# Kernel optimization log

Measured on AMD Instinct MI355X. Metric: run time of the kernel, lower is better.

## Reference

```python
import jax, jax.numpy as jnp
import numpy as np

BINS = 5
POINTS = 2
EPS_DIV = 1e-6
GN_GROUPS = 32
GN_EPS = 1e-5


def bilinear_sum(img, ys, xs):
    """Sum of bilinear samples with zero padding outside the image.
    img: (B, C, H, W); ys, xs: (B, K, H, W) absolute sample coords.
    Returns (B, C, H, W) = sum over K of bilinear(img, ys_k, xs_k)."""
    B, C, H, W = img.shape
    K = ys.shape[1]
    y0 = jnp.floor(ys)
    x0 = jnp.floor(xs)
    imgf = img.reshape(B, C, H * W)
    acc = jnp.zeros((B, C, K, H, W), img.dtype)
    for dy, dx in ((0, 0), (0, 1), (1, 0), (1, 1)):
        yi = y0 + dy
        xi = x0 + dx
        w = (1.0 - jnp.abs(ys - yi)) * (1.0 - jnp.abs(xs - xi))
        valid = (yi >= 0) & (yi <= H - 1) & (xi >= 0) & (xi <= W - 1)
        yc = jnp.clip(yi, 0, H - 1).astype(jnp.int32)
        xc = jnp.clip(xi, 0, W - 1).astype(jnp.int32)
        idx = (yc * W + xc).reshape(B, 1, K * H * W)
        g = jnp.take_along_axis(imgf, idx, axis=2).reshape(B, C, K, H, W)
        acc = acc + (w * valid.astype(img.dtype))[:, None] * g
    return acc.sum(axis=2)


def setup_inputs():
    key = jax.random.key(0)
    ks = jax.random.split(key, 6)
    B, C, H, W = 2, 256, 100, 152
    P, K = POINTS, BINS
    x = jax.random.normal(ks[0], (B, C, H, W), jnp.float32)
    offsets = jax.random.normal(ks[1], (B, P * K * 2, H, W), jnp.float32) * 2.0
    ef_w = jax.random.normal(ks[2], (P * C, C), jnp.float32) * 0.02
    ef_b = jnp.zeros((P * C,), jnp.float32)
    hm1_w = jax.random.normal(ks[3], (P, C, C), jnp.float32) * 0.02
    hm1_b = jnp.zeros((P, C), jnp.float32)
    hm2_w = jax.random.normal(ks[4], (P, C), jnp.float32) * 0.02
    hm2_b = jnp.zeros((P,), jnp.float32)
    merge_w = jax.random.normal(ks[5], (C, P * C), jnp.float32) * 0.02
    merge_b = jnp.zeros((C,), jnp.float32)
    gn_g = jnp.ones((C,), jnp.float32)
    gn_b = jnp.zeros((C,), jnp.float32)
    return {"x": x, "offsets": offsets, "ef_w": ef_w, "ef_b": ef_b,
            "hm1_w": hm1_w, "hm1_b": hm1_b, "hm2_w": hm2_w, "hm2_b": hm2_b,
            "merge_w": merge_w, "merge_b": merge_b, "gn_g": gn_g, "gn_b": gn_b}


def reference(x, offsets, ef_w, ef_b, hm1_w, hm1_b, hm2_w, hm2_b, merge_w, merge_b, gn_g, gn_b):
    B, C, H, W = x.shape
    P, K = POINTS, BINS
    # expand_feat: 1x1 conv C -> P*C
    ef = jnp.einsum('bchw,dc->bdhw', x, ef_w) + ef_b[None, :, None, None]
    efp = ef.reshape(B, P, C, H, W)
    # heatmap: grouped 1x1 conv (per-point) -> ReLU -> grouped 1x1 conv -> exp
    h = jax.nn.relu(jnp.einsum('bpchw,pdc->bpdhw', efp, hm1_w) + hm1_b[None, :, :, None, None])
    heat = jnp.exp(jnp.einsum('bpdhw,pd->bphw', h, hm2_w) + hm2_b[None, :, None, None])  # (B,P,H,W)
    # offsets: (B, P, K, 2, H, W) with channel layout [y, x] per bin.
    # base_offset cancels the [1,bins] kernel grid, so the deform conv with
    # all-ones weights is simply: sum over bins of bilinear samples at
    # (h + off_y, w + off_x).
    off = offsets.reshape(B, P, K, 2, H, W)
    hg = jnp.arange(H, dtype=x.dtype)[None, None, None, :, None]
    wg = jnp.arange(W, dtype=x.dtype)[None, None, None, None, :]
    ys = hg + off[:, :, :, 0]  # (B,P,K,H,W)
    xs = wg + off[:, :, :, 1]
    outs = []
    for p in range(P):
        # sample feat*heat (C channels) and heat (1 channel) together
        img = jnp.concatenate([efp[:, p] * heat[:, p][:, None], heat[:, p][:, None]], axis=1)
        s = bilinear_sum(img, ys[:, p], xs[:, p])  # (B, C+1, H, W)
        outs.append(s[:, :C] / (s[:, C:] + EPS_DIV))
    outs = jnp.concatenate(outs, axis=1)  # (B, P*C, H, W)
    merged = jnp.einsum('bchw,dc->bdhw', outs, merge_w) + merge_b[None, :, None, None]
    # GroupNorm(32, C) + ReLU
    g = merged.reshape(B, GN_GROUPS, C // GN_GROUPS, H, W)
    mu = g.mean(axis=(2, 3, 4), keepdims=True)
    var = g.var(axis=(2, 3, 4), keepdims=True)
    gn = ((g - mu) / jnp.sqrt(var + GN_EPS)).reshape(B, C, H, W)
    gn = gn * gn_g[None, :, None, None] + gn_b[None, :, None, None]
    return jax.nn.relu(gn)
```

## Files before the change

### kernel.cpp

```cpp
#include <hip/hip_runtime.h>

#define BINS 5
#define PTS  2
constexpr int Bx = 2, Cc = 256, Hh = 100, Ww = 152;
constexpr int HW = Hh * Ww;
constexpr int NTILE = 238;
constexpr float EPS_DIV = 1e-6f;
constexpr float GN_EPS  = 1e-5f;

typedef __attribute__((ext_vector_type(8))) _Float16 hfrag;
typedef __attribute__((ext_vector_type(2))) _Float16 h2;
typedef __attribute__((ext_vector_type(4))) float f32x4;

__device__ __forceinline__ ushort f2h(float f) {
    return __builtin_bit_cast(ushort, (_Float16)f);
}
__device__ __forceinline__ float hlo(unsigned u) {
    return (float)__builtin_bit_cast(_Float16, (ushort)(u & 0xffffu));
}
__device__ __forceinline__ float hhi(unsigned u) {
    return (float)__builtin_bit_cast(_Float16, (ushort)(u >> 16));
}

#define GLL16(g, l) __builtin_amdgcn_global_load_lds( \
    (const __attribute__((address_space(1))) unsigned*)(g), \
    (__attribute__((address_space(3))) unsigned*)(l), 16, 0, 0)

__global__ __launch_bounds__(256)
void k_wconv(const float* __restrict__ efw, const float* __restrict__ w1,
             const float* __restrict__ mw, ushort* __restrict__ wb)
{
    int gid = blockIdx.x * 256 + threadIdx.x;
    int e = gid * 4;
    int arr = e >> 17, off = e & 131071;
    const float* src = arr == 0 ? efw : (arr == 1 ? w1 : mw);
    float4 v = *(const float4*)(src + off);
    ushort4 o = { f2h(v.x), f2h(v.y), f2h(v.z), f2h(v.w) };
    *(ushort4*)(wb + e) = o;
}

__global__ __launch_bounds__(256)
void k_xt(const float* __restrict__ x, ushort* __restrict__ xbt)
{
    __shared__ float tile[32][33];
    const int t = threadIdx.x;
    const int hw0 = blockIdx.x * 32;
    const int c0 = blockIdx.y * 32;
    const int b = blockIdx.z;
    const float* xb = x + ((size_t)b * Cc + c0) * HW + hw0;
    const int tx = t & 31, ty = t >> 5;
    #pragma unroll
    for (int r = 0; r < 4; r++) {
        int c = ty + r * 8;
        tile[c][tx] = xb[(size_t)c * HW + tx];
    }
    __syncthreads();
    const int hwl = t >> 3, c4 = (t & 7) * 4;
    ushort4 o = { f2h(tile[c4 + 0][hwl]), f2h(tile[c4 + 1][hwl]),
                  f2h(tile[c4 + 2][hwl]), f2h(tile[c4 + 3][hwl]) };
    *(ushort4*)&xbt[((size_t)b * HW + hw0 + hwl) * Cc + c0 + c4] = o;
}

__global__ __launch_bounds__(512)
void k_ef(const ushort* __restrict__ xbt, const ushort* __restrict__ wbe,
          const float* __restrict__ efb, ushort* __restrict__ efp)
{
    __shared__ ushort Alds[128 * 256];
    __shared__ ushort Bl0[64 * 256];
    __shared__ ushort Bl1[64 * 256];
    const int t  = threadIdx.x;
    const int wv = t >> 6, ln = t & 63;
    const int quad = ln >> 4, l16 = ln & 15;
    const int mwv = wv & 3, ngr = wv >> 2;
    const int xr = l16 & 7;
    const int bx = blockIdx.x;
    const int n0 = blockIdx.y;
    const int b  = blockIdx.z;
    const ushort* xb = xbt + (size_t)b * HW * Cc;
    const ushort* wA = wbe + (size_t)n0 * 128 * 256;
    const int ntl = (237 - bx) / 30 + 1;

    #pragma unroll
    for (int j = 0; j < 8; j++) {
        int unit = j * 512 + t;
        int row = unit >> 5, c8 = unit & 31;
        const ushort* g = wA + row * 256 + ((c8 ^ (row & 7)) << 3);
        ushort* l = Alds + (j * 512 + wv * 64) * 8;
        GLL16(g, l);
    }
    auto stageB = [&](int tt, ushort* dst) {
        int tp0 = tt * 64;
        #pragma unroll
        for (int j = 0; j < 4; j++) {
            int unit = j * 512 + t;
            int prow = unit >> 5, c8 = unit & 31;
            int pq = tp0 + prow; if (pq > HW - 1) pq = HW - 1;
            const ushort* g = xb + (size_t)pq * 256 + ((c8 ^ (prow & 7)) << 3);
            ushort* l = dst + (j * 512 + wv * 64) * 8;
            GLL16(g, l);
        }
    };
    stageB(bx, Bl0);
    stageB(bx + 30, Bl1);
    asm volatile("s_waitcnt vmcnt(4)" ::: "memory");
    __builtin_amdgcn_s_barrier();
    __builtin_amdgcn_sched_barrier(0);

    float bias[2][4];
    #pragma unroll
    for (int dt = 0; dt < 2; dt++)
        #pragma unroll
        for (int r = 0; r < 4; r++)
            bias[dt][r] = efb[n0 * 128 + mwv * 32 + dt * 16 + quad * 4 + r];

    const int aof0 = (mwv * 32 + l16) * 256;
    const int aof1 = (mwv * 32 + 16 + l16) * 256;
    const int bof0 = (ngr * 32 + l16) * 256;
    const int bof1 = (ngr * 32 + 16 + l16) * 256;
    const int p_ = n0 >> 1;
    const int cb = (n0 & 1) * 128 + mwv * 32;
    ushort* outb = efp + (size_t)((b * PTS + p_) * HW) * Cc;

    for (int it = 0; it < ntl; it++) {
        const int tp0 = (bx + it * 30) * 64;
        const ushort* bb = (it & 1) ? Bl1 : Bl0;
        f32x4 acc[2][2];
        #pragma unroll
        for (int i = 0; i < 2; i++)
            #pragma unroll
            for (int j = 0; j < 2; j++) acc[i][j] = (f32x4){0.f, 0.f, 0.f, 0.f};
        #pragma unroll
        for (int s = 0; s < 8; s++) {
            const int co = (((s * 4 + quad) ^ xr) << 3);
            hfrag a0 = *(const hfrag*)&Alds[aof0 + co];
            hfrag a1 = *(const hfrag*)&Alds[aof1 + co];
            hfrag b0 = *(const hfrag*)&bb[bof0 + co];
            hfrag b1 = *(const hfrag*)&bb[bof1 + co];
            acc[0][0] = __builtin_amdgcn_mfma_f32_16x16x32_f16(a0, b0, acc[0][0], 0, 0, 0);
            acc[0][1] = __builtin_amdgcn_mfma_f32_16x16x32_f16(a0, b1, acc[0][1], 0, 0, 0);
            acc[1][0] = __builtin_amdgcn_mfma_f32_16x16x32_f16(a1, b0, acc[1][0], 0, 0, 0);
            acc[1][1] = __builtin_amdgcn_mfma_f32_16x16x32_f16(a1, b1, acc[1][1], 0, 0, 0);
        }
        #pragma unroll
        for (int dt = 0; dt < 2; dt++)
            #pragma unroll
            for (int pt = 0; pt < 2; pt++) {
                int pix = tp0 + ngr * 32 + pt * 16 + l16;
                if (pix < HW) {
                    ushort4 o = { f2h(acc[dt][pt][0] + bias[dt][0]),
                                  f2h(acc[dt][pt][1] + bias[dt][1]),
                                  f2h(acc[dt][pt][2] + bias[dt][2]),
                                  f2h(acc[dt][pt][3] + bias[dt][3]) };
                    *(ushort4*)&outb[(size_t)pix * Cc + cb + dt * 16 + quad * 4] = o;
                }
            }
        if (it + 1 < ntl) {
            __builtin_amdgcn_s_barrier();
            if (it + 2 < ntl) {
                stageB(bx + (it + 2) * 30, (it & 1) ? Bl1 : Bl0);
                asm volatile("s_waitcnt vmcnt(4)" ::: "memory");
            } else {
                asm volatile("s_waitcnt vmcnt(0)" ::: "memory");
            }
            __builtin_amdgcn_s_barrier();
            __builtin_amdgcn_sched_barrier(0);
        }
    }
}

__global__ __launch_bounds__(512)
void k_heat(const ushort* __restrict__ efp, const ushort* __restrict__ wb1,
            const float* __restrict__ b1, const float* __restrict__ w2,
            float* __restrict__ hp)
{
    __shared__ ushort Alds[128 * 256];
    __shared__ ushort Bl0[64 * 256];
    __shared__ ushort Bl1[64 * 256];
    __shared__ float red[2][4][32];
    const int t  = threadIdx.x;
    const int wv = t >> 6, ln = t & 63;
    const int quad = ln >> 4, l16 = ln & 15;
    const int mwv = wv & 3, ngr = wv >> 2;
    const int xr = l16 & 7;
    const int bx = blockIdx.x;
    const int p  = blockIdx.y >> 1;
    const int n0 = blockIdx.y & 1;
    const int b  = blockIdx.z;
    const ushort* eb = efp + (size_t)((b * PTS + p) * HW) * Cc;
    const ushort* wA = wb1 + (size_t)p * Cc * Cc + (size_t)n0 * 128 * 256;
    const int ntl = (237 - bx) / 30 + 1;

    #pragma unroll
    for (int j = 0; j < 8; j++) {
        int unit = j * 512 + t;
        int row = unit >> 5, c8 = unit & 31;
        const ushort* g = wA + row * 256 + ((c8 ^ (row & 7)) << 3);
        ushort* l = Alds + (j * 512 + wv * 64) * 8;
        GLL16(g, l);
    }
    auto stageB = [&](int tt, ushort* dst) {
        int tp0 = tt * 64;
        #pragma unroll
        for (int j = 0; j < 4; j++) {
            int unit = j * 512 + t;
            int prow = unit >> 5, c8 = unit & 31;
            int pq = tp0 + prow; if (pq > HW - 1) pq = HW - 1;
            const ushort* g = eb + (size_t)pq * 256 + ((c8 ^ (prow & 7)) << 3);
            ushort* l = dst + (j * 512 + wv * 64) * 8;
            GLL16(g, l);
        }
    };
    stageB(bx, Bl0);
    stageB(bx + 30, Bl1);
    asm volatile("s_waitcnt vmcnt(4)" ::: "memory");
    __builtin_amdgcn_s_barrier();
    __builtin_amdgcn_sched_barrier(0);

    const float* b1p = b1 + p * 256;
    const float* w2p = w2 + p * 256;
    float b1v[2][4], w2v[2][4];
    #pragma unroll
    for (int dt = 0; dt < 2; dt++)
        #pragma unroll
        for (int r = 0; r < 4; r++) {
            int gch = n0 * 128 + mwv * 32 + dt * 16 + quad * 4 + r;
            b1v[dt][r] = b1p[gch];
            w2v[dt][r] = w2p[gch];
        }

    const int aof0 = (mwv * 32 + l16) * 256;
    const int aof1 = (mwv * 32 + 16 + l16) * 256;
    const int bof0 = (ngr * 32 + l16) * 256;
    const int bof1 = (ngr * 32 + 16 + l16) * 256;
    float* hpo = hp + (size_t)n0 * (Bx * PTS * HW) + (size_t)(b * PTS + p) * HW;

    for (int it = 0; it < ntl; it++) {
        const int tp0 = (bx + it * 30) * 64;
        const ushort* bb = (it & 1) ? Bl1 : Bl0;
        f32x4 acc[2][2];
        #pragma unroll
        for (int i = 0; i < 2; i++)
            #pragma unroll
            for (int j = 0; j < 2; j++) acc[i][j] = (f32x4){0.f, 0.f, 0.f, 0.f};
        #pragma unroll
        for (int s = 0; s < 8; s++) {
            const int co = (((s * 4 + quad) ^ xr) << 3);
            hfrag a0 = *(const hfrag*)&Alds[aof0 + co];
            hfrag a1 = *(const hfrag*)&Alds[aof1 + co];
            hfrag b0 = *(const hfrag*)&bb[bof0 + co];
            hfrag b1f = *(const hfrag*)&bb[bof1 + co];
            acc[0][0] = __builtin_amdgcn_mfma_f32_16x16x32_f16(a0, b0, acc[0][0], 0, 0, 0);
            acc[0][1] = __builtin_amdgcn_mfma_f32_16x16x32_f16(a0, b1f, acc[0][1], 0, 0, 0);
            acc[1][0] = __builtin_amdgcn_mfma_f32_16x16x32_f16(a1, b0, acc[1][0], 0, 0, 0);
            acc[1][1] = __builtin_amdgcn_mfma_f32_16x16x32_f16(a1, b1f, acc[1][1], 0, 0, 0);
        }
        float s0 = 0.f, s1 = 0.f;
        #pragma unroll
        for (int dt = 0; dt < 2; dt++)
            #pragma unroll
            for (int r = 0; r < 4; r++) {
                float h0 = acc[dt][0][r] + b1v[dt][r];
                float h1 = acc[dt][1][r] + b1v[dt][r];
                h0 = h0 > 0.f ? h0 : 0.f;
                h1 = h1 > 0.f ? h1 : 0.f;
                s0 += w2v[dt][r] * h0;
                s1 += w2v[dt][r] * h1;
            }
        s0 += __shfl_xor(s0, 16); s0 += __shfl_xor(s0, 32);
        s1 += __shfl_xor(s1, 16); s1 += __shfl_xor(s1, 32);
        if (ln < 16) {
            red[ngr][mwv][ln]      = s0;
            red[ngr][mwv][16 + ln] = s1;
        }
        asm volatile("s_waitcnt lgkmcnt(0)" ::: "memory");
        __builtin_amdgcn_s_barrier();
        if (t < 64) {
            int g = t >> 5, i32 = t & 31;
            float v = red[g][0][i32] + red[g][1][i32] + red[g][2][i32] + red[g][3][i32];
            int pix = tp0 + t;
            if (pix < HW) hpo[pix] = v;
        }
        if (it + 1 < ntl) {
            if (it + 2 < ntl) {
                stageB(bx + (it + 2) * 30, (it & 1) ? Bl1 : Bl0);
                asm volatile("s_waitcnt vmcnt(4)" ::: "memory");
            } else {
                asm volatile("s_waitcnt vmcnt(0)" ::: "memory");
            }
            __builtin_amdgcn_s_barrier();
            __builtin_amdgcn_sched_barrier(0);
        }
    }
}

__global__ __launch_bounds__(256)
void k_hexp(const float* __restrict__ hp, const float* __restrict__ b2,
            float* __restrict__ heat)
{
    int t4 = blockIdx.x * 256 + threadIdx.x;
    if (t4 >= (Bx * PTS * HW) / 4) return;
    int i = t4 * 4;
    float b2v = b2[(i / HW) & 1];
    float4 a = *(const float4*)(hp + i);
    float4 c = *(const float4*)(hp + (size_t)(Bx * PTS * HW) + i);
    float4 o;
    o.x = expf(a.x + c.x + b2v);
    o.y = expf(a.y + c.y + b2v);
    o.z = expf(a.z + c.z + b2v);
    o.w = expf(a.w + c.w + b2v);
    *(float4*)(heat + i) = o;
}

__global__ __launch_bounds__(256)
void k_sample(const ushort* __restrict__ efp, const float* __restrict__ heat,
              const float* __restrict__ offs, ushort* __restrict__ outs)
{
    __shared__ uint2 s_wo[32][20];
    const int t = threadIdx.x;
    const int bid = blockIdx.x;
    const int nx = (bid & 7) * 60 + (bid >> 3);
    if (nx >= 475) return;
    const int m0 = nx * 32;
    const int p = blockIdx.y;
    const int b = blockIdx.z;
    const float* heat_bp = heat + (size_t)(b * PTS + p) * HW;

    if (t < 32 * BINS) {
        int j = t / BINS, k = t % BINS;
        int hw = m0 + j;
        int hh = hw / Ww, ww = hw % Ww;
        int chy = (p * BINS + k) * 2;
        float oy = offs[((size_t)b * (PTS * BINS * 2) + chy)     * HW + hw];
        float ox = offs[((size_t)b * (PTS * BINS * 2) + chy + 1) * HW + hw];
        float ysf = (float)hh + oy;
        float xsf = (float)ww + ox;
        float y0 = floorf(ysf), x0 = floorf(xsf);
        #pragma unroll
        for (int dy = 0; dy < 2; dy++)
            #pragma unroll
            for (int dx = 0; dx < 2; dx++) {
                float yi = y0 + dy, xi = x0 + dx;
                float wgt = (1.f - fabsf(ysf - yi)) * (1.f - fabsf(xsf - xi));
                bool valid = (yi >= 0.f) && (yi <= (float)(Hh - 1)) &&
                             (xi >= 0.f) && (xi <= (float)(Ww - 1));
                int yc = (int)yi; yc = yc < 0 ? 0 : (yc > Hh - 1 ? Hh - 1 : yc);
                int xc = (int)xi; xc = xc < 0 ? 0 : (xc > Ww - 1 ? Ww - 1 : xc);
                int idx = yc * Ww + xc;
                float wh = valid ? wgt * heat_bp[idx] : 0.f;
                s_wo[j][k * 4 + dy * 2 + dx] =
                    make_uint2(__float_as_uint(wh), (unsigned)idx << 9);
            }
    }
    __syncthreads();
    if (t < 32) {
        float s = 0.f;
        #pragma unroll
        for (int u = 0; u < 20; u++) s += __uint_as_float(s_wo[t][u].x);
        float inv = 1.f / (s + EPS_DIV);
        #pragma unroll
        for (int u = 0; u < 20; u++) {
            float w = __uint_as_float(s_wo[t][u].x) * inv;
            unsigned hw16 = (unsigned)f2h(w);
            s_wo[t][u].x = hw16 | (hw16 << 16);
        }
    }
    __syncthreads();

    const int wv = t >> 6, ln = t & 63;
    const int half = ln >> 5, c8 = ln & 31;
    const char* efbase = (const char*)(efp + (size_t)((b * PTS + p) * HW) * Cc)
                         + c8 * 16;
    ushort* ob = outs + ((size_t)(b * HW + m0)) * (PTS * Cc) + p * Cc + c8 * 8;
    #pragma unroll
    for (int i = 0; i < 8; i += 2) {
        const int j = wv * 8 + i + half;
        h2 a0 = (h2){0, 0}, a1 = (h2){0, 0}, a2 = (h2){0, 0}, a3 = (h2){0, 0};
        #pragma unroll
        for (int u = 0; u < 20; u++) {
            uint2 wo = s_wo[j][u];
            uint4 v = *(const uint4*)(efbase + wo.y);
            h2 wp = __builtin_bit_cast(h2, wo.x);
            a0 += wp * __builtin_bit_cast(h2, v.x);
            a1 += wp * __builtin_bit_cast(h2, v.y);
            a2 += wp * __builtin_bit_cast(h2, v.z);
            a3 += wp * __builtin_bit_cast(h2, v.w);
        }
        uint4 o = { __builtin_bit_cast(unsigned, a0), __builtin_bit_cast(unsigned, a1),
                    __builtin_bit_cast(unsigned, a2), __builtin_bit_cast(unsigned, a3) };
        *(uint4*)(ob + (size_t)j * (PTS * Cc)) = o;
    }
}

__global__ __launch_bounds__(256)
void k_merge(const ushort* __restrict__ outs, const ushort* __restrict__ wbm,
             const float* __restrict__ mb, ushort* __restrict__ mgb,
             float* __restrict__ part2)
{
    __shared__ ushort As[64 * 72];
    __shared__ ushort Bs[64 * 72];
    const int t = threadIdx.x;
    const int wv = t >> 6, ln = t & 63;
    const int quad = ln >> 4, l16 = ln & 15;
    const int pix0 = blockIdx.x * 64;
    const int n0 = blockIdx.y * 64;
    const int b = blockIdx.z;
    const ushort* ob = outs + (size_t)b * HW * (PTS * Cc);

    f32x4 acc[4];
    #pragma unroll
    for (int j = 0; j < 4; j++) acc[j] = (f32x4){0.f, 0.f, 0.f, 0.f};

    const int srow = t >> 3, scol = (t & 7) * 8;

    for (int k0 = 0; k0 < 512; k0 += 64) {
        #pragma unroll
        for (int r = 0; r < 2; r++) {
            int row = srow + r * 32;
            *(uint4*)&As[row * 72 + scol] =
                *(const uint4*)&wbm[(size_t)(n0 + row) * 512 + k0 + scol];
        }
        #pragma unroll
        for (int r = 0; r < 2; r++) {
            int row = srow + r * 32;
            int pq = pix0 + row; if (pq > HW - 1) pq = HW - 1;
            *(uint4*)&Bs[row * 72 + scol] =
                *(const uint4*)&ob[(size_t)pq * (PTS * Cc) + k0 + scol];
        }
        __syncthreads();
        #pragma unroll
        for (int kk = 0; kk < 64; kk += 32) {
            hfrag af = *(const hfrag*)&As[(wv * 16 + l16) * 72 + kk + quad * 8];
            #pragma unroll
            for (int pt = 0; pt < 4; pt++) {
                hfrag bfr = *(const hfrag*)&Bs[(pt * 16 + l16) * 72 + kk + quad * 8];
                acc[pt] = __builtin_amdgcn_mfma_f32_16x16x32_f16(
                    af, bfr, acc[pt], 0, 0, 0);
            }
        }
        __syncthreads();
    }

    const int ch = n0 + wv * 16 + quad * 4;
    float bias[4];
    #pragma unroll
    for (int r = 0; r < 4; r++) bias[r] = mb[ch + r];

    float sacc = 0.f, qacc = 0.f;
    #pragma unroll
    for (int pt = 0; pt < 4; pt++) {
        int pix = pix0 + pt * 16 + l16;
        if (pix < HW) {
            #pragma unroll
            for (int r = 0; r < 4; r++) {
                float v = acc[pt][r] + bias[r];
                mgb[((size_t)b * Cc + ch + r) * HW + pix] = f2h(v);
                sacc += v; qacc += v * v;
            }
        }
    }
    #pragma unroll
    for (int off = 1; off <= 16; off <<= 1) {
        sacc += __shfl_xor(sacc, off);
        qacc += __shfl_xor(qacc, off);
    }
    if ((ln & 31) == 0) {
        int g = (n0 >> 3) + wv * 2 + (quad >> 1);
        size_t idx = ((size_t)(b * 32 + g) * NTILE + blockIdx.x) * 2;
        part2[idx + 0] = sacc;
        part2[idx + 1] = qacc;
    }
}

__global__ __launch_bounds__(256)
void k_gnfinal(const float* __restrict__ part2, float* __restrict__ statf)
{
    const int bg = blockIdx.x;
    const int t = threadIdx.x;
    float s = 0.f, q = 0.f;
    if (t < NTILE) {
        s = part2[((size_t)bg * NTILE + t) * 2 + 0];
        q = part2[((size_t)bg * NTILE + t) * 2 + 1];
    }
    #pragma unroll
    for (int off = 1; off <= 32; off <<= 1) {
        s += __shfl_xor(s, off);
        q += __shfl_xor(q, off);
    }
    __shared__ float rs[4], rq[4];
    int wid = t >> 6;
    if ((t & 63) == 0) { rs[wid] = s; rq[wid] = q; }
    __syncthreads();
    if (t == 0) {
        float S = rs[0] + rs[1] + rs[2] + rs[3];
        float Q = rq[0] + rq[1] + rq[2] + rq[3];
        const float n = 8.f * HW;
        float mean = S / n;
        float var  = Q / n - mean * mean;
        statf[bg * 2 + 0] = mean;
        statf[bg * 2 + 1] = rsqrtf(var + GN_EPS);
    }
}

__global__ __launch_bounds__(256)
void k_gnapply(const ushort* __restrict__ mgb, const float* __restrict__ statf,
               const float* __restrict__ gg, const float* __restrict__ gb,
               float* __restrict__ out)
{
    const int i8 = blockIdx.x * 256 + threadIdx.x;
    const int i = i8 * 8;
    const int CHW = Cc * HW;
    const int b = i / CHW;
    const int r = i - b * CHW;
    const int c = r / HW;
    const int g = c >> 3;
    float mean = statf[(b * 32 + g) * 2 + 0];
    float istd = statf[(b * 32 + g) * 2 + 1];
    float sc = istd * gg[c];
    float sh = gb[c] - mean * sc;
    uint4 v = *(const uint4*)(mgb + i);
    float4 o0, o1;
    o0.x = fmaxf(hlo(v.x) * sc + sh, 0.f);
    o0.y = fmaxf(hhi(v.x) * sc + sh, 0.f);
    o0.z = fmaxf(hlo(v.y) * sc + sh, 0.f);
    o0.w = fmaxf(hhi(v.y) * sc + sh, 0.f);
    o1.x = fmaxf(hlo(v.z) * sc + sh, 0.f);
    o1.y = fmaxf(hhi(v.z) * sc + sh, 0.f);
    o1.z = fmaxf(hlo(v.w) * sc + sh, 0.f);
    o1.w = fmaxf(hhi(v.w) * sc + sh, 0.f);
    *(float4*)(out + i)     = o0;
    *(float4*)(out + i + 4) = o1;
}

extern "C" void kernel_launch(void* const* d_in, const int* in_sizes, int n_in,
                              void* d_out, int out_size, void* d_ws, size_t ws_size,
                              hipStream_t stream)
{
    const float* x    = (const float*)d_in[0];
    const float* offs = (const float*)d_in[1];
    const float* efw  = (const float*)d_in[2];
    const float* efb  = (const float*)d_in[3];
    const float* w1   = (const float*)d_in[4];
    const float* b1   = (const float*)d_in[5];
    const float* w2   = (const float*)d_in[6];
    const float* b2   = (const float*)d_in[7];
    const float* mw   = (const float*)d_in[8];
    const float* mb   = (const float*)d_in[9];
    const float* gg   = (const float*)d_in[10];
    const float* gb   = (const float*)d_in[11];
    float* out = (float*)d_out;

    ushort* wb    = (ushort*)d_ws;
    ushort* wbe   = wb;
    ushort* wb1   = wb + 131072;
    ushort* wbm   = wb + 262144;
    ushort* efp   = wb + 393216;
    ushort* outsb = efp + (size_t)Bx * PTS * HW * Cc;
    ushort* xbt   = outsb + (size_t)Bx * HW * PTS * Cc;
    ushort* mgb   = xbt + (size_t)Bx * HW * Cc;
    float*  heat  = (float*)(mgb + (size_t)Bx * Cc * HW);
    float*  part2 = heat + (size_t)Bx * PTS * HW;
    float*  statf = part2 + (size_t)64 * NTILE * 2;
    float*  hp    = statf + 128;

    dim3 blk(256);
    k_wconv  <<<dim3(384),              blk, 0, stream>>>(efw, w1, mw, wb);
    k_xt     <<<dim3(475, 8, Bx),       blk, 0, stream>>>(x, xbt);
    k_ef     <<<dim3(30, 4, Bx),  dim3(512), 0, stream>>>(xbt, wbe, efb, efp);
    k_heat   <<<dim3(30, 4, Bx),  dim3(512), 0, stream>>>(efp, wb1, b1, w2, hp);
    k_hexp   <<<dim3(60),               blk, 0, stream>>>(hp, b2, heat);
    k_sample <<<dim3(480, PTS, Bx),     blk, 0, stream>>>(efp, heat, offs, outsb);
    k_merge  <<<dim3(NTILE, 4, Bx),     blk, 0, stream>>>(outsb, wbm, mb, mgb, part2);
    k_gnfinal<<<dim3(64),               blk, 0, stream>>>(part2, statf);
    k_gnapply<<<dim3(Bx * Cc * HW / 8 / 256), blk, 0, stream>>>(mgb, statf, gg, gb, out);
}
```

Measured before the change: 209.3 us.

## Hold GEMM weights in registers with 32x32 MFMA, fuse heat exp, reorganize tiling

The weight-conversion kernel now writes weights pre-swizzled into MFMA 32x32x16 fragment order. The three GEMM kernels (expand, heat, merge) then load their A operand straight into registers instead of staging it through LDS. Each block handles all output channels for two 64-pixel tiles, and the merge kernel switches from a 256-thread LDS-tiled loop to this double-buffered layout. The heat kernel also folds the exp and bias step in, which removes the separate k_hexp launch and the partial heat buffer. The cost is high register pressure (up to 32 fragments per thread), and each block now computes only two tiles, so there is less load/compute overlap than the earlier persistent loop.

```diff
diff --git a/kernel.cpp b/kernel.cpp
--- a/kernel.cpp
+++ b/kernel.cpp
@@ -8,9 +8,9 @@
 constexpr float EPS_DIV = 1e-6f;
 constexpr float GN_EPS  = 1e-5f;
 
-typedef __attribute__((ext_vector_type(8))) _Float16 hfrag;
-typedef __attribute__((ext_vector_type(2))) _Float16 h2;
-typedef __attribute__((ext_vector_type(4))) float f32x4;
+typedef __attribute__((ext_vector_type(8)))  _Float16 hfrag;
+typedef __attribute__((ext_vector_type(2)))  _Float16 h2;
+typedef __attribute__((ext_vector_type(16))) float    f32x16;
 
 __device__ __forceinline__ ushort f2h(float f) {
     return __builtin_bit_cast(ushort, (_Float16)f);
@@ -26,17 +26,34 @@
     (const __attribute__((address_space(1))) unsigned*)(g), \
     (__attribute__((address_space(3))) unsigned*)(l), 16, 0, 0)
 
+#define MFMA32(a, b, c) __builtin_amdgcn_mfma_f32_32x32x16_f16(a, b, c, 0, 0, 0)
+
 __global__ __launch_bounds__(256)
 void k_wconv(const float* __restrict__ efw, const float* __restrict__ w1,
              const float* __restrict__ mw, ushort* __restrict__ wb)
 {
     int gid = blockIdx.x * 256 + threadIdx.x;
-    int e = gid * 4;
-    int arr = e >> 17, off = e & 131071;
+    int i = gid * 8;
+    int arr = i >> 17, off = i & 131071;
     const float* src = arr == 0 ? efw : (arr == 1 ? w1 : mw);
-    float4 v = *(const float4*)(src + off);
-    ushort4 o = { f2h(v.x), f2h(v.y), f2h(v.z), f2h(v.w) };
-    *(ushort4*)(wb + e) = o;
+    float4 v0 = *(const float4*)(src + off);
+    float4 v1 = *(const float4*)(src + off + 4);
+    int outaddr;
+    if (arr == 0) {
+        int m = off >> 8, k = off & 255;
+        outaddr = (((k >> 4) * 16 + (m >> 5)) * 64 + (m & 31) + 32 * ((k >> 3) & 1)) * 8;
+    } else if (arr == 1) {
+        int p = off >> 16, r = off & 65535;
+        int m = r >> 8, k = r & 255;
+        outaddr = p * 65536 +
+                  (((k >> 4) * 8 + (m >> 5)) * 64 + (m & 31) + 32 * ((k >> 3) & 1)) * 8;
+    } else {
+        int m = off >> 9, k = off & 511;
+        outaddr = (((k >> 4) * 8 + (m >> 5)) * 64 + (m & 31) + 32 * ((k >> 3) & 1)) * 8;
+    }
+    ushort o[8] = { f2h(v0.x), f2h(v0.y), f2h(v0.z), f2h(v0.w),
+                    f2h(v1.x), f2h(v1.y), f2h(v1.z), f2h(v1.w) };
+    *(uint4*)(wb + arr * 131072 + outaddr) = *(uint4*)o;
 }
 
 __global__ __launch_bounds__(256)
@@ -61,33 +78,27 @@
     *(ushort4*)&xbt[((size_t)b * HW + hw0 + hwl) * Cc + c0 + c4] = o;
 }
 
-__global__ __launch_bounds__(512)
+__global__ __launch_bounds__(512, 2)
 void k_ef(const ushort* __restrict__ xbt, const ushort* __restrict__ wbe,
           const float* __restrict__ efb, ushort* __restrict__ efp)
 {
-    __shared__ ushort Alds[128 * 256];
-    __shared__ ushort Bl0[64 * 256];
-    __shared__ ushort Bl1[64 * 256];
-    const int t  = threadIdx.x;
+    __shared__ ushort B0[64 * 256];
+    __shared__ ushort B1[64 * 256];
+    const int t = threadIdx.x;
     const int wv = t >> 6, ln = t & 63;
-    const int quad = ln >> 4, l16 = ln & 15;
-    const int mwv = wv & 3, ngr = wv >> 2;
-    const int xr = l16 & 7;
-    const int bx = blockIdx.x;
-    const int n0 = blockIdx.y;
-    const int b  = blockIdx.z;
+    const int l31 = ln & 31, lh = ln >> 5;
+    const int b = blockIdx.y;
+    const int tt0 = blockIdx.x * 2;
     const ushort* xb = xbt + (size_t)b * HW * Cc;
-    const ushort* wA = wbe + (size_t)n0 * 128 * 256;
-    const int ntl = (237 - bx) / 30 + 1;
-
+
+    hfrag A[2][16];
     #pragma unroll
-    for (int j = 0; j < 8; j++) {
-        int unit = j * 512 + t;
-        int row = unit >> 5, c8 = unit & 31;
-        const ushort* g = wA + row * 256 + ((c8 ^ (row & 7)) << 3);
-        ushort* l = Alds + (j * 512 + wv * 64) * 8;
-        GLL16(g, l);
-    }
+    for (int mf = 0; mf < 2; mf++)
+        #pragma unroll
+        for (int ks = 0; ks < 16; ks++)
+            A[mf][ks] = *(const hfrag*)&wbe[((ks * 16 + (wv * 2 + mf)) * 64 + ln) * 8];
+    __builtin_amdgcn_sched_barrier(0);
+
     auto stageB = [&](int tt, ushort* dst) {
         int tp0 = tt * 64;
         #pragma unroll
@@ -95,109 +106,93 @@
             int unit = j * 512 + t;
             int prow = unit >> 5, c8 = unit & 31;
             int pq = tp0 + prow; if (pq > HW - 1) pq = HW - 1;
-            const ushort* g = xb + (size_t)pq * 256 + ((c8 ^ (prow & 7)) << 3);
+            const ushort* g = xb + (size_t)pq * Cc + ((c8 ^ (prow & 7)) << 3);
             ushort* l = dst + (j * 512 + wv * 64) * 8;
             GLL16(g, l);
         }
     };
-    stageB(bx, Bl0);
-    stageB(bx + 30, Bl1);
+    stageB(tt0, B0);
+    stageB(tt0 + 1, B1);
+    __builtin_amdgcn_sched_barrier(0);
     asm volatile("s_waitcnt vmcnt(4)" ::: "memory");
     __builtin_amdgcn_s_barrier();
     __builtin_amdgcn_sched_barrier(0);
 
-    float bias[2][4];
-    #pragma unroll
-    for (int dt = 0; dt < 2; dt++)
-        #pragma unroll
-        for (int r = 0; r < 4; r++)
-            bias[dt][r] = efb[n0 * 128 + mwv * 32 + dt * 16 + quad * 4 + r];
-
-    const int aof0 = (mwv * 32 + l16) * 256;
-    const int aof1 = (mwv * 32 + 16 + l16) * 256;
-    const int bof0 = (ngr * 32 + l16) * 256;
-    const int bof1 = (ngr * 32 + 16 + l16) * 256;
-    const int p_ = n0 >> 1;
-    const int cb = (n0 & 1) * 128 + mwv * 32;
-    ushort* outb = efp + (size_t)((b * PTS + p_) * HW) * Cc;
-
-    for (int it = 0; it < ntl; it++) {
-        const int tp0 = (bx + it * 30) * 64;
-        const ushort* bb = (it & 1) ? Bl1 : Bl0;
-        f32x4 acc[2][2];
-        #pragma unroll
-        for (int i = 0; i < 2; i++)
-            #pragma unroll
-            for (int j = 0; j < 2; j++) acc[i][j] = (f32x4){0.f, 0.f, 0.f, 0.f};
-        #pragma unroll
-        for (int s = 0; s < 8; s++) {
-            const int co = (((s * 4 + quad) ^ xr) << 3);
-            hfrag a0 = *(const hfrag*)&Alds[aof0 + co];
-            hfrag a1 = *(const hfrag*)&Alds[aof1 + co];
-            hfrag b0 = *(const hfrag*)&bb[bof0 + co];
-            hfrag b1 = *(const hfrag*)&bb[bof1 + co];
-            acc[0][0] = __builtin_amdgcn_mfma_f32_16x16x32_f16(a0, b0, acc[0][0], 0, 0, 0);
-            acc[0][1] = __builtin_amdgcn_mfma_f32_16x16x32_f16(a0, b1, acc[0][1], 0, 0, 0);
-            acc[1][0] = __builtin_amdgcn_mfma_f32_16x16x32_f16(a1, b0, acc[1][0], 0, 0, 0);
-            acc[1][1] = __builtin_amdgcn_mfma_f32_16x16x32_f16(a1, b1, acc[1][1], 0, 0, 0);
-        }
-        #pragma unroll
-        for (int dt = 0; dt < 2; dt++)
-            #pragma unroll
-            for (int pt = 0; pt < 2; pt++) {
-                int pix = tp0 + ngr * 32 + pt * 16 + l16;
-                if (pix < HW) {
-                    ushort4 o = { f2h(acc[dt][pt][0] + bias[dt][0]),
-                                  f2h(acc[dt][pt][1] + bias[dt][1]),
-                                  f2h(acc[dt][pt][2] + bias[dt][2]),
-                                  f2h(acc[dt][pt][3] + bias[dt][3]) };
-                    *(ushort4*)&outb[(size_t)pix * Cc + cb + dt * 16 + quad * 4] = o;
+    auto compute = [&](int tt, const ushort* Bs) {
+        f32x16 acc[2][2];
+        #pragma unroll
+        for (int mf = 0; mf < 2; mf++)
+            #pragma unroll
+            for (int pf = 0; pf < 2; pf++)
+                #pragma unroll
+                for (int r = 0; r < 16; r++) acc[mf][pf][r] = 0.f;
+        #pragma unroll
+        for (int ks = 0; ks < 16; ks++) {
+            int c = ks * 2 + lh;
+            #pragma unroll
+            for (int pf = 0; pf < 2; pf++) {
+                hfrag bf = *(const hfrag*)&Bs[(pf * 32 + l31) * 256 + ((c ^ (l31 & 7)) << 3)];
+                acc[0][pf] = MFMA32(A[0][ks], bf, acc[0][pf]);
+                acc[1][pf] = MFMA32(A[1][ks], bf, acc[1][pf]);
+            }
+        }
+        const int tp0 = tt * 64;
+        const int p_ = wv >> 2;
+        ushort* outb = efp + (size_t)((b * PTS + p_) * HW) * Cc;
+        #pragma unroll
+        for (int mf = 0; mf < 2; mf++) {
+            int m0 = wv * 2 + mf;
+            int chb = (m0 * 32) & 255;
+            #pragma unroll
+            for (int q = 0; q < 4; q++) {
+                float4 bv = *(const float4*)&efb[m0 * 32 + q * 8 + 4 * lh];
+                #pragma unroll
+                for (int pf = 0; pf < 2; pf++) {
+                    int px = tp0 + pf * 32 + l31;
+                    if (px < HW) {
+                        int ch = chb + q * 8 + 4 * lh;
+                        ushort4 o = { f2h(acc[mf][pf][q * 4 + 0] + bv.x),
+                                      f2h(acc[mf][pf][q * 4 + 1] + bv.y),
+                                      f2h(acc[mf][pf][q * 4 + 2] + bv.z),
+                                      f2h(acc[mf][pf][q * 4 + 3] + bv.w) };
+                        *(ushort4*)&outb[(size_t)px * Cc + ch] = o;
+                    }
                 }
             }
-        if (it + 1 < ntl) {
-            __builtin_amdgcn_s_barrier();
-            if (it + 2 < ntl) {
-                stageB(bx + (it + 2) * 30, (it & 1) ? Bl1 : Bl0);
-                asm volatile("s_waitcnt vmcnt(4)" ::: "memory");
-            } else {
-                asm volatile("s_waitcnt vmcnt(0)" ::: "memory");
-            }
-            __builtin_amdgcn_s_barrier();
-            __builtin_amdgcn_sched_barrier(0);
-        }
-    }
-}
-
-__global__ __launch_bounds__(512)
+        }
+    };
+    compute(tt0, B0);
+    asm volatile("s_waitcnt vmcnt(0)" ::: "memory");
+    __builtin_amdgcn_s_barrier();
+    __builtin_amdgcn_sched_barrier(0);
+    compute(tt0 + 1, B1);
+}
+
+__global__ __launch_bounds__(512, 2)
 void k_heat(const ushort* __restrict__ efp, const ushort* __restrict__ wb1,
             const float* __restrict__ b1, const float* __restrict__ w2,
-            float* __restrict__ hp)
-{
-    __shared__ ushort Alds[128 * 256];
-    __shared__ ushort Bl0[64 * 256];
-    __shared__ ushort Bl1[64 * 256];
-    __shared__ float red[2][4][32];
-    const int t  = threadIdx.x;
+            const float* __restrict__ b2, float* __restrict__ heat)
+{
+    __shared__ ushort B0[64 * 256];
+    __shared__ ushort B1[64 * 256];
+    __shared__ float red[8][64];
+    const int t = threadIdx.x;
     const int wv = t >> 6, ln = t & 63;
-    const int quad = ln >> 4, l16 = ln & 15;
-    const int mwv = wv & 3, ngr = wv >> 2;
-    const int xr = l16 & 7;
-    const int bx = blockIdx.x;
-    const int p  = blockIdx.y >> 1;
-    const int n0 = blockIdx.y & 1;
-    const int b  = blockIdx.z;
+    const int l31 = ln & 31, lh = ln >> 5;
+    const int zz = blockIdx.y;
+    const int b = zz >> 1, p = zz & 1;
+    const int tt0 = blockIdx.x * 2;
     const ushort* eb = efp + (size_t)((b * PTS + p) * HW) * Cc;
-    const ushort* wA = wb1 + (size_t)p * Cc * Cc + (size_t)n0 * 128 * 256;
-    const int ntl = (237 - bx) / 30 + 1;
-
+    const float* b1p = b1 + p * 256;
+    const float* w2p = w2 + p * 256;
+    const float b2v = b2[p];
+
+    hfrag A[16];
     #pragma unroll
-    for (int j = 0; j < 8; j++) {
-        int unit = j * 512 + t;
-        int row = unit >> 5, c8 = unit & 31;
-        const ushort* g = wA + row * 256 + ((c8 ^ (row & 7)) << 3);
-        ushort* l = Alds + (j * 512 + wv * 64) * 8;
-        GLL16(g, l);
-    }
+    for (int ks = 0; ks < 16; ks++)
+        A[ks] = *(const hfrag*)&wb1[p * 65536 + ((ks * 8 + wv) * 64 + ln) * 8];
+    __builtin_amdgcn_sched_barrier(0);
+
     auto stageB = [&](int tt, ushort* dst) {
         int tp0 = tt * 64;
         #pragma unroll
@@ -205,110 +200,70 @@
             int unit = j * 512 + t;
             int prow = unit >> 5, c8 = unit & 31;
             int pq = tp0 + prow; if (pq > HW - 1) pq = HW - 1;
-            const ushort* g = eb + (size_t)pq * 256 + ((c8 ^ (prow & 7)) << 3);
+            const ushort* g = eb + (size_t)pq * Cc + ((c8 ^ (prow & 7)) << 3);
             ushort* l = dst + (j * 512 + wv * 64) * 8;
             GLL16(g, l);
         }
     };
-    stageB(bx, Bl0);
-    stageB(bx + 30, Bl1);
+    stageB(tt0, B0);
+    stageB(tt0 + 1, B1);
+    __builtin_amdgcn_sched_barrier(0);
     asm volatile("s_waitcnt vmcnt(4)" ::: "memory");
     __builtin_amdgcn_s_barrier();
     __builtin_amdgcn_sched_barrier(0);
 
-    const float* b1p = b1 + p * 256;
-    const float* w2p = w2 + p * 256;
-    float b1v[2][4], w2v[2][4];
-    #pragma unroll
-    for (int dt = 0; dt < 2; dt++)
-        #pragma unroll
-        for (int r = 0; r < 4; r++) {
-            int gch = n0 * 128 + mwv * 32 + dt * 16 + quad * 4 + r;
-            b1v[dt][r] = b1p[gch];
-            w2v[dt][r] = w2p[gch];
-        }
-
-    const int aof0 = (mwv * 32 + l16) * 256;
-    const int aof1 = (mwv * 32 + 16 + l16) * 256;
-    const int bof0 = (ngr * 32 + l16) * 256;
-    const int bof1 = (ngr * 32 + 16 + l16) * 256;
-    float* hpo = hp + (size_t)n0 * (Bx * PTS * HW) + (size_t)(b * PTS + p) * HW;
-
-    for (int it = 0; it < ntl; it++) {
-        const int tp0 = (bx + it * 30) * 64;
-        const ushort* bb = (it & 1) ? Bl1 : Bl0;
-        f32x4 acc[2][2];
-        #pragma unroll
-        for (int i = 0; i < 2; i++)
-            #pragma unroll
-            for (int j = 0; j < 2; j++) acc[i][j] = (f32x4){0.f, 0.f, 0.f, 0.f};
-        #pragma unroll
-        for (int s = 0; s < 8; s++) {
-            const int co = (((s * 4 + quad) ^ xr) << 3);
-            hfrag a0 = *(const hfrag*)&Alds[aof0 + co];
-            hfrag a1 = *(const hfrag*)&Alds[aof1 + co];
-            hfrag b0 = *(const hfrag*)&bb[bof0 + co];
-            hfrag b1f = *(const hfrag*)&bb[bof1 + co];
-            acc[0][0] = __builtin_amdgcn_mfma_f32_16x16x32_f16(a0, b0, acc[0][0], 0, 0, 0);
-            acc[0][1] = __builtin_amdgcn_mfma_f32_16x16x32_f16(a0, b1f, acc[0][1], 0, 0, 0);
-            acc[1][0] = __builtin_amdgcn_mfma_f32_16x16x32_f16(a1, b0, acc[1][0], 0, 0, 0);
-            acc[1][1] = __builtin_amdgcn_mfma_f32_16x16x32_f16(a1, b1f, acc[1][1], 0, 0, 0);
-        }
-        float s0 = 0.f, s1 = 0.f;
-        #pragma unroll
-        for (int dt = 0; dt < 2; dt++)
-            #pragma unroll
-            for (int r = 0; r < 4; r++) {
-                float h0 = acc[dt][0][r] + b1v[dt][r];
-                float h1 = acc[dt][1][r] + b1v[dt][r];
-                h0 = h0 > 0.f ? h0 : 0.f;
-                h1 = h1 > 0.f ? h1 : 0.f;
-                s0 += w2v[dt][r] * h0;
-                s1 += w2v[dt][r] * h1;
-            }
-        s0 += __shfl_xor(s0, 16); s0 += __shfl_xor(s0, 32);
-        s1 += __shfl_xor(s1, 16); s1 += __shfl_xor(s1, 32);
-        if (ln < 16) {
-            red[ngr][mwv][ln]      = s0;
-            red[ngr][mwv][16 + ln] = s1;
+    auto compute = [&](int tt, const ushort* Bs) {
+        f32x16 acc[2];
+        #pragma unroll
+        for (int pf = 0; pf < 2; pf++)
+            #pragma unroll
+            for (int r = 0; r < 16; r++) acc[pf][r] = 0.f;
+        #pragma unroll
+        for (int ks = 0; ks < 16; ks++) {
+            int c = ks * 2 + lh;
+            #pragma unroll
+            for (int pf = 0; pf < 2; pf++) {
+                hfrag bf = *(const hfrag*)&Bs[(pf * 32 + l31) * 256 + ((c ^ (l31 & 7)) << 3)];
+                acc[pf] = MFMA32(A[ks], bf, acc[pf]);
+            }
+        }
+        float s[2] = {0.f, 0.f};
+        #pragma unroll
+        for (int q = 0; q < 4; q++) {
+            float4 b1v = *(const float4*)&b1p[wv * 32 + q * 8 + 4 * lh];
+            float4 w2v = *(const float4*)&w2p[wv * 32 + q * 8 + 4 * lh];
+            #pragma unroll
+            for (int pf = 0; pf < 2; pf++) {
+                float h0 = acc[pf][q * 4 + 0] + b1v.x;
+                float h1 = acc[pf][q * 4 + 1] + b1v.y;
+                float h2_ = acc[pf][q * 4 + 2] + b1v.z;
+                float h3 = acc[pf][q * 4 + 3] + b1v.w;
+                s[pf] += w2v.x * (h0 > 0.f ? h0 : 0.f);
+                s[pf] += w2v.y * (h1 > 0.f ? h1 : 0.f);
+                s[pf] += w2v.z * (h2_ > 0.f ? h2_ : 0.f);
+                s[pf] += w2v.w * (h3 > 0.f ? h3 : 0.f);
+            }
+        }
+        s[0] += __shfl_xor(s[0], 32);
+        s[1] += __shfl_xor(s[1], 32);
+        if (lh == 0) {
+            red[wv][l31]      = s[0];
+            red[wv][32 + l31] = s[1];
         }
         asm volatile("s_waitcnt lgkmcnt(0)" ::: "memory");
         __builtin_amdgcn_s_barrier();
         if (t < 64) {
-            int g = t >> 5, i32 = t & 31;
-            float v = red[g][0][i32] + red[g][1][i32] + red[g][2][i32] + red[g][3][i32];
-            int pix = tp0 + t;
-            if (pix < HW) hpo[pix] = v;
-        }
-        if (it + 1 < ntl) {
-            if (it + 2 < ntl) {
-                stageB(bx + (it + 2) * 30, (it & 1) ? Bl1 : Bl0);
-                asm volatile("s_waitcnt vmcnt(4)" ::: "memory");
-            } else {
-                asm volatile("s_waitcnt vmcnt(0)" ::: "memory");
-            }
-            __builtin_amdgcn_s_barrier();
-            __builtin_amdgcn_sched_barrier(0);
-        }
-    }
-}
-
-__global__ __launch_bounds__(256)
-void k_hexp(const float* __restrict__ hp, const float* __restrict__ b2,
-            float* __restrict__ heat)
-{
-    int t4 = blockIdx.x * 256 + threadIdx.x;
-    if (t4 >= (Bx * PTS * HW) / 4) return;
-    int i = t4 * 4;
-    float b2v = b2[(i / HW) & 1];
-    float4 a = *(const float4*)(hp + i);
-    float4 c = *(const float4*)(hp + (size_t)(Bx * PTS * HW) + i);
-    float4 o;
-    o.x = expf(a.x + c.x + b2v);
-    o.y = expf(a.y + c.y + b2v);
-    o.z = expf(a.z + c.z + b2v);
-    o.w = expf(a.w + c.w + b2v);
-    *(float4*)(heat + i) = o;
+            float v = red[0][t] + red[1][t] + red[2][t] + red[3][t] +
+                      red[4][t] + red[5][t] + red[6][t] + red[7][t];
+            int px = tt * 64 + t;
+            if (px < HW) heat[(size_t)(b * PTS + p) * HW + px] = expf(v + b2v);
+        }
+    };
+    compute(tt0, B0);
+    asm volatile("s_waitcnt vmcnt(0)" ::: "memory");
+    __builtin_amdgcn_s_barrier();
+    __builtin_amdgcn_sched_barrier(0);
+    compute(tt0 + 1, B1);
 }
 
 __global__ __launch_bounds__(256)
@@ -391,84 +346,104 @@
     }
 }
 
-__global__ __launch_bounds__(256)
+__global__ __launch_bounds__(512, 2)
 void k_merge(const ushort* __restrict__ outs, const ushort* __restrict__ wbm,
              const float* __restrict__ mb, ushort* __restrict__ mgb,
              float* __restrict__ part2)
 {
-    __shared__ ushort As[64 * 72];
-    __shared__ ushort Bs[64 * 72];
+    __shared__ ushort B0[64 * 512];
+    __shared__ ushort B1[64 * 512];
     const int t = threadIdx.x;
     const int wv = t >> 6, ln = t & 63;
-    const int quad = ln >> 4, l16 = ln & 15;
-    const int pix0 = blockIdx.x * 64;
-    const int n0 = blockIdx.y * 64;
-    const int b = blockIdx.z;
+    const int l31 = ln & 31, lh = ln >> 5;
+    const int b = blockIdx.y;
+    const int tt0 = blockIdx.x * 2;
     const ushort* ob = outs + (size_t)b * HW * (PTS * Cc);
 
-    f32x4 acc[4];
+    hfrag A[32];
     #pragma unroll
-    for (int j = 0; j < 4; j++) acc[j] = (f32x4){0.f, 0.f, 0.f, 0.f};
-
-    const int srow = t >> 3, scol = (t & 7) * 8;
-
-    for (int k0 = 0; k0 < 512; k0 += 64) {
-        #pragma unroll
-        for (int r = 0; r < 2; r++) {
-            int row = srow + r * 32;
-            *(uint4*)&As[row * 72 + scol] =
-                *(const uint4*)&wbm[(size_t)(n0 + row) * 512 + k0 + scol];
-        }
-        #pragma unroll
-        for (int r = 0; r < 2; r++) {
-            int row = srow + r * 32;
-            int pq = pix0 + row; if (pq > HW - 1) pq = HW - 1;
-            *(uint4*)&Bs[row * 72 + scol] =
-                *(const uint4*)&ob[(size_t)pq * (PTS * Cc) + k0 + scol];
-        }
-        __syncthreads();
-        #pragma unroll
-        for (int kk = 0; kk < 64; kk += 32) {
-            hfrag af = *(const hfrag*)&As[(wv * 16 + l16) * 72 + kk + quad * 8];
-            #pragma unroll
-            for (int pt = 0; pt < 4; pt++) {
-                hfrag bfr = *(const hfrag*)&Bs[(pt * 16 + l16) * 72 + kk + quad * 8];
-                acc[pt] = __builtin_amdgcn_mfma_f32_16x16x32_f16(
-                    af, bfr, acc[pt], 0, 0, 0);
-            }
-        }
-        __syncthreads();
-    }
-
-    const int ch = n0 + wv * 16 + quad * 4;
-    float bias[4];
-    #pragma unroll
-    for (int r = 0; r < 4; r++) bias[r] = mb[ch + r];
-
-    float sacc = 0.f, qacc = 0.f;
-    #pragma unroll
-    for (int pt = 0; pt < 4; pt++) {
-        int pix = pix0 + pt * 16 + l16;
-        if (pix < HW) {
-            #pragma unroll
-            for (int r = 0; r < 4; r++) {
-                float v = acc[pt][r] + bias[r];
-                mgb[((size_t)b * Cc + ch + r) * HW + pix] = f2h(v);
-                sacc += v; qacc += v * v;
-            }
-        }
-    }
-    #pragma unroll
-    for (int off = 1; off <= 16; off <<= 1) {
-        sacc += __shfl_xor(sacc, off);
-        qacc += __shfl_xor(qacc, off);
-    }
-    if ((ln & 31) == 0) {
-        int g = (n0 >> 3) + wv * 2 + (quad >> 1);
-        size_t idx = ((size_t)(b * 32 + g) * NTILE + blockIdx.x) * 2;
-        part2[idx + 0] = sacc;
-        part2[idx + 1] = qacc;
-    }
+    for (int ks = 0; ks < 32; ks++)
+        A[ks] = *(const hfrag*)&wbm[((ks * 8 + wv) * 64 + ln) * 8];
+    __builtin_amdgcn_sched_barrier(0);
+
+    auto stageB = [&](int tt, ushort* dst) {
+        int tp0 = tt * 64;
+        #pragma unroll
+        for (int j = 0; j < 8; j++) {
+            int unit = j * 512 + t;
+            int prow = unit >> 6, c8 = unit & 63;
+            int pq = tp0 + prow; if (pq > HW - 1) pq = HW - 1;
+            const ushort* g = ob + (size_t)pq * (PTS * Cc) + ((c8 ^ (prow & 7)) << 3);
+            ushort* l = dst + (j * 512 + wv * 64) * 8;
+            GLL16(g, l);
+        }
+    };
+    stageB(tt0, B0);
+    stageB(tt0 + 1, B1);
+    __builtin_amdgcn_sched_barrier(0);
+    asm volatile("s_waitcnt vmcnt(8)" ::: "memory");
+    __builtin_amdgcn_s_barrier();
+    __builtin_amdgcn_sched_barrier(0);
+
+    auto compute = [&](int tt, const ushort* Bs) {
+        f32x16 acc[2];
+        #pragma unroll
+        for (int pf = 0; pf < 2; pf++)
+            #pragma unroll
+            for (int r = 0; r < 16; r++) acc[pf][r] = 0.f;
+        #pragma unroll
+        for (int ks = 0; ks < 32; ks++) {
+            int c = ks * 2 + lh;
+            #pragma unroll
+            for (int pf = 0; pf < 2; pf++) {
+                hfrag bf = *(const hfrag*)&Bs[(pf * 32 + l31) * 512 + ((c ^ (l31 & 7)) << 3)];
+                acc[pf] = MFMA32(A[ks], bf, acc[pf]);
+            }
+        }
+        const int tp0 = tt * 64;
+        float sg[4] = {0.f, 0.f, 0.f, 0.f};
+        float qg[4] = {0.f, 0.f, 0.f, 0.f};
+        #pragma unroll
+        for (int q = 0; q < 4; q++) {
+            float4 bv = *(const float4*)&mb[wv * 32 + q * 8 + 4 * lh];
+            #pragma unroll
+            for (int pf = 0; pf < 2; pf++) {
+                int px = tp0 + pf * 32 + l31;
+                if (px < HW) {
+                    #pragma unroll
+                    for (int r = 0; r < 4; r++) {
+                        float bb = r == 0 ? bv.x : (r == 1 ? bv.y : (r == 2 ? bv.z : bv.w));
+                        float v = acc[pf][q * 4 + r] + bb;
+                        int ch = wv * 32 + q * 8 + 4 * lh + r;
+                        mgb[((size_t)b * Cc + ch) * HW + px] = f2h(v);
+                        sg[q] += v; qg[q] += v * v;
+                    }
+                }
+            }
+        }
+        #pragma unroll
+        for (int q = 0; q < 4; q++) {
+            #pragma unroll
+            for (int off = 1; off <= 32; off <<= 1) {
+                sg[q] += __shfl_xor(sg[q], off);
+                qg[q] += __shfl_xor(qg[q], off);
+            }
+        }
+        if (ln == 0) {
+            #pragma unroll
+            for (int q = 0; q < 4; q++) {
+                int g = wv * 4 + q;
+                size_t idx = ((size_t)(b * 32 + g) * NTILE + tt) * 2;
+                part2[idx + 0] = sg[q];
+                part2[idx + 1] = qg[q];
+            }
+        }
+    };
+    compute(tt0, B0);
+    asm volatile("s_waitcnt vmcnt(0)" ::: "memory");
+    __builtin_amdgcn_s_barrier();
+    __builtin_amdgcn_sched_barrier(0);
+    compute(tt0 + 1, B1);
 }
 
 __global__ __launch_bounds__(256)
@@ -560,16 +535,14 @@
     float*  heat  = (float*)(mgb + (size_t)Bx * Cc * HW);
     float*  part2 = heat + (size_t)Bx * PTS * HW;
     float*  statf = part2 + (size_t)64 * NTILE * 2;
-    float*  hp    = statf + 128;
 
     dim3 blk(256);
-    k_wconv  <<<dim3(384),              blk, 0, stream>>>(efw, w1, mw, wb);
+    k_wconv  <<<dim3(192),              blk, 0, stream>>>(efw, w1, mw, wb);
     k_xt     <<<dim3(475, 8, Bx),       blk, 0, stream>>>(x, xbt);
-    k_ef     <<<dim3(30, 4, Bx),  dim3(512), 0, stream>>>(xbt, wbe, efb, efp);
-    k_heat   <<<dim3(30, 4, Bx),  dim3(512), 0, stream>>>(efp, wb1, b1, w2, hp);
-    k_hexp   <<<dim3(60),               blk, 0, stream>>>(hp, b2, heat);
+    k_ef     <<<dim3(119, Bx),    dim3(512), 0, stream>>>(xbt, wbe, efb, efp);
+    k_heat   <<<dim3(119, 4),     dim3(512), 0, stream>>>(efp, wb1, b1, w2, b2, heat);
     k_sample <<<dim3(480, PTS, Bx),     blk, 0, stream>>>(efp, heat, offs, outsb);
-    k_merge  <<<dim3(NTILE, 4, Bx),     blk, 0, stream>>>(outsb, wbm, mb, mgb, part2);
+    k_merge  <<<dim3(119, Bx),    dim3(512), 0, stream>>>(outsb, wbm, mb, mgb, part2);
     k_gnfinal<<<dim3(64),               blk, 0, stream>>>(part2, statf);
     k_gnapply<<<dim3(Bx * Cc * HW / 8 / 256), blk, 0, stream>>>(mgb, statf, gg, gb, out);
 }
```

Result: no change. 206.3 us (-1.4%).
